# Performance work log

Measured on AMD Instinct MI355X. Metric: run time of the kernel, lower is better.

Reference implementation:

```python
import jax, jax.numpy as jnp
import numpy as np

B, S, D, H = 2, 2048, 768, 12
DK = D // H
NEG = -1000000000.0


def setup_inputs() -> dict:
    key = jax.random.key(0)
    ks = jax.random.split(key, 12)
    inp = {
        "query": jax.random.normal(ks[0], (B, S, D), jnp.float32),
        "key": jax.random.normal(ks[1], (B, S, D), jnp.float32),
        "value": jax.random.normal(ks[2], (B, S, D), jnp.float32),
        "mask": jax.random.randint(ks[3], (B, 1, 1, S), 0, 2, jnp.int32),
    }
    sc = 1.0 / np.sqrt(D)
    inp["Wq"] = jax.random.normal(ks[4], (D, D), jnp.float32) * sc
    inp["bq"] = jnp.zeros((D,), jnp.float32)
    inp["Wk"] = jax.random.normal(ks[5], (D, D), jnp.float32) * sc
    inp["bk"] = jnp.zeros((D,), jnp.float32)
    inp["Wv"] = jax.random.normal(ks[6], (D, D), jnp.float32) * sc
    inp["bv"] = jnp.zeros((D,), jnp.float32)
    inp["Wo"] = jax.random.normal(ks[7], (D, D), jnp.float32) * sc
    inp["bo"] = jnp.zeros((D,), jnp.float32)
    return inp


def reference(query, key, value, mask, Wq, bq, Wk, bk, Wv, bv, Wo, bo):
    b = query.shape[0]
    # QKV projections -> [B, H, S, DK]
    def proj(x, W, bias):
        y = jnp.einsum('bsd,de->bse', x, W.T) + bias
        return y.reshape(b, -1, H, DK).transpose(0, 2, 1, 3)
    q = proj(query, Wq, bq)
    k = proj(key, Wk, bk)
    v = proj(value, Wv, bv)
    # scores: [B, H, S, S]
    scores = jnp.einsum('bhqd,bhkd->bhqk', q, k) / jnp.sqrt(jnp.float32(DK))
    scores = jnp.where(mask == 0, jnp.float32(NEG), scores)
    p = jax.nn.softmax(scores, axis=-1)
    x = jnp.einsum('bhqk,bhkd->bhqd', p, v)  # [B, H, S, DK]
    x = x.transpose(0, 2, 1, 3).reshape(b, -1, H * DK)
    return jnp.einsum('bsd,de->bse', x, Wo.T) + bo
```

## Files before the change

kernel.cpp:

```cpp
#include <hip/hip_runtime.h>

typedef unsigned short u16;
typedef __attribute__((ext_vector_type(8))) __bf16 bf16x8;
typedef __attribute__((ext_vector_type(8))) short s16x8;
typedef __attribute__((ext_vector_type(8))) unsigned short u16x8;
typedef __attribute__((ext_vector_type(4))) float f32x4;
typedef __attribute__((ext_vector_type(4))) unsigned short u16x4;
typedef __attribute__((ext_vector_type(4))) float fl4;
typedef __attribute__((ext_vector_type(4))) int i32x4;
typedef __attribute__((ext_vector_type(4))) unsigned char u8x4;

#define MFMA(a, b, c) __builtin_amdgcn_mfma_f32_16x16x32_bf16((a), (b), (c), 0, 0, 0)
#define QSC 0.18033688011112042f

__device__ __forceinline__ u16 f2bf(float f) {
  __bf16 h = (__bf16)f;
  return __builtin_bit_cast(unsigned short, h);
}

__device__ __forceinline__ float bf2f(u16 u) {
  union { unsigned u; float f; } v; v.u = ((unsigned)u) << 16;
  return v.f;
}

__device__ __forceinline__ void gll16(const u16* g, u16* l) {
  typedef __attribute__((address_space(1))) unsigned int gu32;
  typedef __attribute__((address_space(3))) unsigned int lu32;
  __builtin_amdgcn_global_load_lds((gu32*)g, (lu32*)l, 16, 0, 0);
}


__global__ __launch_bounds__(256) void k_convert_w(
    const float* __restrict__ Wq, const float* __restrict__ Wk,
    const float* __restrict__ Wv, const float* __restrict__ Wo,
    u16* __restrict__ wqkv, u16* __restrict__ wob) {
  const int n = 3072 * 192;
  for (int i = blockIdx.x * 256 + threadIdx.x; i < n; i += gridDim.x * 256) {
    int row = i / 192;
    int col = (i - row * 192) * 4;
    const float* src; u16* dst; float sc = 1.0f;
    if (row < 768)       { src = Wq + row * 768;          dst = wqkv + row * 768; sc = QSC; }
    else if (row < 1536) { src = Wk + (row - 768) * 768;  dst = wqkv + row * 768; }
    else if (row < 2304) { src = Wv + (row - 1536) * 768; dst = wqkv + row * 768; }
    else                 { src = Wo + (row - 2304) * 768; dst = wob + (row - 2304) * 768; }
    fl4 f = *(const fl4*)(src + col);
    u16x4 o;
    o[0] = f2bf(f[0] * sc); o[1] = f2bf(f[1] * sc);
    o[2] = f2bf(f[2] * sc); o[3] = f2bf(f[3] * sc);
    *(u16x4*)(dst + col) = o;
  }
}


__global__ __launch_bounds__(256) void k_gemm_qkv(
    const float* __restrict__ xq, const float* __restrict__ xk,
    const float* __restrict__ xv, const u16* __restrict__ wqkv,
    const float* __restrict__ bq, const float* __restrict__ bk_,
    const float* __restrict__ bv_,
    u16* __restrict__ Qb, u16* __restrict__ Kb, u16* __restrict__ Vtb) {
  __shared__ __align__(16) u16 Abuf[2][128 * 32];
  __shared__ __align__(16) u16 Bbuf[2][128 * 32];
  const int tid = threadIdx.x;
  const int row0 = blockIdx.x * 128, col0 = blockIdx.y * 128;
  const int seg = col0 / 768;
  const float* A32 = (seg == 0) ? xq : ((seg == 1) ? xk : xv);
  const int w = tid >> 6, lane = tid & 63, lr = lane & 15, kg = lane >> 4;
  const int wr = (w >> 1) * 64, wc = (w & 1) * 64;

  const int c0 = tid, c1 = tid + 256;
  const int r0c = c0 >> 2, g0 = (c0 & 3) ^ ((r0c >> 1) & 3);
  const int r1c = c1 >> 2, g1 = (c1 & 3) ^ ((r1c >> 1) & 3);
  const float* aS0 = A32 + (size_t)(row0 + r0c) * 768 + g0 * 8;
  const float* aS1 = A32 + (size_t)(row0 + r1c) * 768 + g1 * 8;
  const u16* bS0 = wqkv + (size_t)(col0 + r0c) * 768 + g0 * 8;
  const u16* bS1 = wqkv + (size_t)(col0 + r1c) * 768 + g1 * 8;

  f32x4 acc[4][4];
  f32x4 zero = {0.f, 0.f, 0.f, 0.f};
#pragma unroll
  for (int i = 0; i < 4; i++)
#pragma unroll
    for (int j = 0; j < 4; j++) acc[i][j] = zero;

  int aoff[4], boff[4];
#pragma unroll
  for (int mi = 0; mi < 4; mi++) {
    int r = wr + mi * 16 + lr;
    aoff[mi] = r * 32 + (kg ^ ((r >> 1) & 3)) * 8;
  }
#pragma unroll
  for (int ni = 0; ni < 4; ni++) {
    int r = wc + ni * 16 + lr;
    boff[ni] = r * 32 + (kg ^ ((r >> 1) & 3)) * 8;
  }

  fl4 ar[4];
#define LOADA(kt) { ar[0] = *(const fl4*)(aS0 + (kt) * 32);       \
                    ar[1] = *(const fl4*)(aS0 + (kt) * 32 + 4);   \
                    ar[2] = *(const fl4*)(aS1 + (kt) * 32);       \
                    ar[3] = *(const fl4*)(aS1 + (kt) * 32 + 4); }
#define WRITEA(buf) { u16x8 t0, t1;                               \
    t0[0]=f2bf(ar[0][0]); t0[1]=f2bf(ar[0][1]); t0[2]=f2bf(ar[0][2]); t0[3]=f2bf(ar[0][3]); \
    t0[4]=f2bf(ar[1][0]); t0[5]=f2bf(ar[1][1]); t0[6]=f2bf(ar[1][2]); t0[7]=f2bf(ar[1][3]); \
    t1[0]=f2bf(ar[2][0]); t1[1]=f2bf(ar[2][1]); t1[2]=f2bf(ar[2][2]); t1[3]=f2bf(ar[2][3]); \
    t1[4]=f2bf(ar[3][0]); t1[5]=f2bf(ar[3][1]); t1[6]=f2bf(ar[3][2]); t1[7]=f2bf(ar[3][3]); \
    *(u16x8*)((buf) + c0 * 8) = t0; *(u16x8*)((buf) + c1 * 8) = t1; }
#define STAGEB(kt, buf) { gll16(bS0 + (kt) * 32, (buf) + c0 * 8); \
                          gll16(bS1 + (kt) * 32, (buf) + c1 * 8); }

  LOADA(0);
  STAGEB(0, Bbuf[0]);
  WRITEA(Abuf[0]);
  __syncthreads();

  for (int kt = 0; kt < 24; kt++) {
    const int cur = kt & 1;
    if (kt < 23) { LOADA(kt + 1); STAGEB(kt + 1, Bbuf[cur ^ 1]); }
    bf16x8 af[4], bfr[4];
#pragma unroll
    for (int mi = 0; mi < 4; mi++) af[mi] = *(const bf16x8*)(Abuf[cur] + aoff[mi]);
#pragma unroll
    for (int ni = 0; ni < 4; ni++) bfr[ni] = *(const bf16x8*)(Bbuf[cur] + boff[ni]);
#pragma unroll
    for (int mi = 0; mi < 4; mi++)
#pragma unroll
      for (int ni = 0; ni < 4; ni++)
        acc[mi][ni] = MFMA(af[mi], bfr[ni], acc[mi][ni]);
    if (kt < 23) WRITEA(Abuf[cur ^ 1]);
    __syncthreads();
  }
#undef LOADA
#undef WRITEA
#undef STAGEB

  const float* bias = (seg == 0) ? bq : ((seg == 1) ? bk_ : bv_);
  const float bsc = (seg == 0) ? QSC : 1.0f;
  const int ncol0 = col0 - seg * 768;
#pragma unroll
  for (int ni = 0; ni < 4; ni++) {
    const int n = ncol0 + wc + ni * 16 + lr;
    const float bval = bias[n] * bsc;
    const int hh = n >> 6, dk = n & 63;
#pragma unroll
    for (int mi = 0; mi < 4; mi++)
#pragma unroll
      for (int j = 0; j < 4; j++) {
        const int m = row0 + wr + mi * 16 + kg * 4 + j;
        const int bb = m >> 11, ss = m & 2047;
        const u16 val = f2bf(acc[mi][ni][j] + bval);
        if (seg == 0)
          Qb[((size_t)((bb * 12 + hh) * 2048 + ss)) * 64 + dk] = val;
        else if (seg == 1)
          Kb[((size_t)((bb * 12 + hh) * 2048 + ss)) * 64 + dk] = val;
        else
          Vtb[((size_t)((bb * 12 + hh) * 64 + dk)) * 2048 + ss] = val;
      }
  }
}


__global__ __launch_bounds__(256) void k_attn(
    const u16* __restrict__ Qb, const u16* __restrict__ Kb,
    const u16* __restrict__ Vtb, const int* __restrict__ mask,
    u16* __restrict__ o_part, float* __restrict__ l_part) {
  __shared__ __align__(16) u16 Ks[2][64 * 64];
  __shared__ __align__(16) u16 Vs[2][64 * 64];
  __shared__ __align__(16) u16 Ps[4][32 * 64];
  __shared__ __align__(4) unsigned char mlds8[1024];
  const int bid = blockIdx.x;
  const int wid = (bid & 7) * 96 + (bid >> 3);
  const int qt = wid & 15;
  const int gh = wid >> 4;
  const int bh = gh >> 1, half = gh & 1;
  const int b = bh / 12;
  const int kvb = half << 10;
  const int tid = threadIdx.x, w = tid >> 6, lane = tid & 63;
  const int lr = lane & 15, g = lane >> 4;
  const int q0 = qt * 128 + w * 32;
  const u16* Qh = Qb + (size_t)bh * (2048 * 64);
  const u16* Kh = Kb + (size_t)bh * (2048 * 64);
  const u16* Vh = Vtb + (size_t)bh * (64 * 2048);
  const int* mb = mask + b * 2048;
  u16* Pw = Ps[w];

  {
    i32x4 m4 = *(const i32x4*)(mb + kvb + tid * 4);
    u8x4 m8;
    m8[0] = (unsigned char)m4[0]; m8[1] = (unsigned char)m4[1];
    m8[2] = (unsigned char)m4[2]; m8[3] = (unsigned char)m4[3];
    *(u8x4*)(mlds8 + tid * 4) = m8;
  }

  bf16x8 aq[2][2];
#pragma unroll
  for (int mi = 0; mi < 2; mi++)
#pragma unroll
    for (int ks = 0; ks < 2; ks++)
      aq[mi][ks] = *(const bf16x8*)(Qh + (q0 + mi * 16 + lr) * 64 + ks * 32 + g * 8);

  f32x4 zero = {0.f, 0.f, 0.f, 0.f};
  f32x4 o[2][4];
#pragma unroll
  for (int mi = 0; mi < 2; mi++)
#pragma unroll
    for (int di = 0; di < 4; di++) o[mi][di] = zero;
  f32x4 o_l[2];
  o_l[0] = zero; o_l[1] = zero;

  s16x8 ov = {0x3F80, 0x3F80, 0x3F80, 0x3F80, 0x3F80, 0x3F80, 0x3F80, 0x3F80};
  bf16x8 ones = __builtin_bit_cast(bf16x8, ov);

  const int c0 = tid, c1 = tid + 256;
  const int sr0 = c0 >> 3, sg0 = (c0 & 7) ^ (sr0 & 7);
  const int sr1 = c1 >> 3, sg1 = (c1 & 7) ^ (sr1 & 7);
  const u16* kA0 = Kh + (size_t)kvb * 64 + sr0 * 64 + sg0 * 8;
  const u16* kA1 = Kh + (size_t)kvb * 64 + sr1 * 64 + sg1 * 8;
  const u16* vA0 = Vh + sr0 * 2048 + kvb + sg0 * 8;
  const u16* vA1 = Vh + sr1 * 2048 + kvb + sg1 * 8;

#define STAGE(u) { u16* kd = Ks[(u)&1]; u16* vd = Vs[(u)&1];           \
    gll16(kA0 + (u) * 4096, kd + c0 * 8);                              \
    gll16(kA1 + (u) * 4096, kd + c1 * 8);                              \
    gll16(vA0 + (u) * 64,  vd + c0 * 8);                               \
    gll16(vA1 + (u) * 64,  vd + c1 * 8); }

  STAGE(0);
  __syncthreads();

  for (int t = 0; t < 16; t++) {
    if (t < 15) STAGE(t + 1);
    const u16* Kc = Ks[t & 1];
    const u16* Vc = Vs[t & 1];

    f32x4 s[2][4];
#pragma unroll
    for (int ni = 0; ni < 4; ni++) {
      const int row = ni * 16 + lr;
      bf16x8 b0 = *(const bf16x8*)(Kc + row * 64 + ((g ^ (row & 7)) << 3));
      bf16x8 b1 = *(const bf16x8*)(Kc + row * 64 + (((4 + g) ^ (row & 7)) << 3));
#pragma unroll
      for (int mi = 0; mi < 2; mi++) {
        f32x4 z = MFMA(b0, aq[mi][0], zero);
        z = MFMA(b1, aq[mi][1], z);
        s[mi][ni] = z;
      }
    }
#pragma unroll
    for (int ni = 0; ni < 4; ni++) {
      const u8x4 mk4 = *(const u8x4*)(mlds8 + t * 64 + ni * 16 + g * 4);
#pragma unroll
      for (int mi = 0; mi < 2; mi++)
#pragma unroll
        for (int j = 0; j < 4; j++)
          s[mi][ni][j] = mk4[j] ? s[mi][ni][j] : -1e9f;
    }

#pragma unroll
    for (int mi = 0; mi < 2; mi++) {
      const int prow = mi * 16 + lr;
      const int rbase = prow * 128, sw = (prow & 7) << 4;
#pragma unroll
      for (int ni = 0; ni < 4; ni++) {
        u16x4 pk;
#pragma unroll
        for (int j = 0; j < 4; j++)
          pk[j] = f2bf(__builtin_amdgcn_exp2f(s[mi][ni][j]));
        *(u16x4*)(Pw + ((rbase + ((ni * 32 + g * 8) ^ sw)) >> 1)) = pk;
      }
    }

#pragma unroll
    for (int ks2 = 0; ks2 < 2; ks2++) {
      bf16x8 ap[2];
#pragma unroll
      for (int mi = 0; mi < 2; mi++) {
        const int prow = mi * 16 + lr;
        const int byt = prow * 128 + ((ks2 * 64 + g * 16) ^ ((prow & 7) << 4));
        ap[mi] = *(const bf16x8*)(Pw + (byt >> 1));
      }
#pragma unroll
      for (int di = 0; di < 4; di++) {
        const int vrow = di * 16 + lr;
        bf16x8 bv = *(const bf16x8*)(Vc + vrow * 64 + (((ks2 * 4 + g) ^ (vrow & 7)) << 3));
#pragma unroll
        for (int mi = 0; mi < 2; mi++)
          o[mi][di] = MFMA(ap[mi], bv, o[mi][di]);
      }
#pragma unroll
      for (int mi = 0; mi < 2; mi++)
        o_l[mi] = MFMA(ap[mi], ones, o_l[mi]);
    }

    if (t < 15) __syncthreads();
  }
#undef STAGE

  u16* opw = o_part + (size_t)(half * 24 + bh) * (2048 * 64);
  float* lpw = l_part + (size_t)(half * 24 + bh) * 2048;
#pragma unroll
  for (int mi = 0; mi < 2; mi++) {
#pragma unroll
    for (int di = 0; di < 4; di++)
#pragma unroll
      for (int j = 0; j < 4; j++) {
        const int row = q0 + mi * 16 + g * 4 + j;
        opw[(size_t)row * 64 + di * 16 + lr] = f2bf(o[mi][di][j]);
      }
    if (lr == 0) {
#pragma unroll
      for (int j = 0; j < 4; j++)
        lpw[q0 + mi * 16 + g * 4 + j] = o_l[mi][j];
    }
  }
}


__global__ __launch_bounds__(256) void k_combine(
    const u16* __restrict__ o_part, const float* __restrict__ l_part,
    u16* __restrict__ attn) {
  const int idx = blockIdx.x * 256 + threadIdx.x;
  const int row = idx >> 3;
  const int c8 = (idx & 7) << 3;
  const size_t HALF_O = (size_t)24 * 2048 * 64;
  u16x8 a0 = *(const u16x8*)(o_part + (size_t)row * 64 + c8);
  u16x8 a1 = *(const u16x8*)(o_part + HALF_O + (size_t)row * 64 + c8);
  const float l = l_part[row] + l_part[24 * 2048 + row];
  const float rcp = 1.0f / l;
  u16x8 r;
#pragma unroll
  for (int j = 0; j < 8; j++)
    r[j] = f2bf((bf2f(a0[j]) + bf2f(a1[j])) * rcp);
  const int bh = row >> 11, s = row & 2047;
  const int b = bh / 12, h = bh - b * 12;
  *(u16x8*)(attn + (size_t)(b * 2048 + s) * 768 + h * 64 + c8) = r;
}


__global__ __launch_bounds__(256) void k_gemm_out(
    const u16* __restrict__ attn, const u16* __restrict__ wob,
    const float* __restrict__ bo, float* __restrict__ out) {
  __shared__ __align__(16) u16 As[2][128 * 32];
  __shared__ __align__(16) u16 Bs[2][128 * 32];
  const int tid = threadIdx.x;
  const int bid = blockIdx.x;
  const int wid = (bid & 7) * 24 + (bid >> 3);
  const int row0 = (wid / 6) * 128, col0 = (wid % 6) * 128;
  const int w = tid >> 6, lane = tid & 63, lr = lane & 15, kg = lane >> 4;
  const int wr = (w >> 1) * 64, wc = (w & 1) * 64;

  const int c0 = tid, c1 = tid + 256;
  const int r0c = c0 >> 2, g0 = (c0 & 3) ^ ((r0c >> 1) & 3);
  const int r1c = c1 >> 2, g1 = (c1 & 3) ^ ((r1c >> 1) & 3);
  const u16* aS0 = attn + (size_t)(row0 + r0c) * 768 + g0 * 8;
  const u16* aS1 = attn + (size_t)(row0 + r1c) * 768 + g1 * 8;
  const u16* bS0 = wob + (size_t)(col0 + r0c) * 768 + g0 * 8;
  const u16* bS1 = wob + (size_t)(col0 + r1c) * 768 + g1 * 8;

  f32x4 acc[4][4];
  f32x4 zero = {0.f, 0.f, 0.f, 0.f};
#pragma unroll
  for (int i = 0; i < 4; i++)
#pragma unroll
    for (int j = 0; j < 4; j++) acc[i][j] = zero;

  int aoff[4], boff[4];
#pragma unroll
  for (int mi = 0; mi < 4; mi++) {
    int r = wr + mi * 16 + lr;
    aoff[mi] = r * 32 + (kg ^ ((r >> 1) & 3)) * 8;
  }
#pragma unroll
  for (int ni = 0; ni < 4; ni++) {
    int r = wc + ni * 16 + lr;
    boff[ni] = r * 32 + (kg ^ ((r >> 1) & 3)) * 8;
  }

#define STAGE(kt) { u16* ad = As[(kt)&1]; u16* bd = Bs[(kt)&1];   \
    gll16(aS0 + (kt) * 32, ad + c0 * 8);                          \
    gll16(aS1 + (kt) * 32, ad + c1 * 8);                          \
    gll16(bS0 + (kt) * 32, bd + c0 * 8);                          \
    gll16(bS1 + (kt) * 32, bd + c1 * 8); }

  STAGE(0);
  __syncthreads();

  for (int kt = 0; kt < 24; kt++) {
    const int cur = kt & 1;
    if (kt < 23) STAGE(kt + 1);
    bf16x8 af[4], bfr[4];
#pragma unroll
    for (int mi = 0; mi < 4; mi++) af[mi] = *(const bf16x8*)(As[cur] + aoff[mi]);
#pragma unroll
    for (int ni = 0; ni < 4; ni++) bfr[ni] = *(const bf16x8*)(Bs[cur] + boff[ni]);
#pragma unroll
    for (int mi = 0; mi < 4; mi++)
#pragma unroll
      for (int ni = 0; ni < 4; ni++)
        acc[mi][ni] = MFMA(af[mi], bfr[ni], acc[mi][ni]);
    if (kt < 23) __syncthreads();
  }
#undef STAGE

#pragma unroll
  for (int ni = 0; ni < 4; ni++) {
    const int n = col0 + wc + ni * 16 + lr;
    const float bval = bo[n];
#pragma unroll
    for (int mi = 0; mi < 4; mi++)
#pragma unroll
      for (int j = 0; j < 4; j++) {
        const int m = row0 + wr + mi * 16 + kg * 4 + j;
        out[(size_t)m * 768 + n] = acc[mi][ni][j] + bval;
      }
  }
}


extern "C" void kernel_launch(void* const* d_in, const int* in_sizes, int n_in,
                              void* d_out, int out_size, void* d_ws, size_t ws_size,
                              hipStream_t stream) {
  const float* q = (const float*)d_in[0];
  const float* k = (const float*)d_in[1];
  const float* v = (const float*)d_in[2];
  const int* mask = (const int*)d_in[3];
  const float* Wq = (const float*)d_in[4];
  const float* bq = (const float*)d_in[5];
  const float* Wk = (const float*)d_in[6];
  const float* bk = (const float*)d_in[7];
  const float* Wv = (const float*)d_in[8];
  const float* bv = (const float*)d_in[9];
  const float* Wo = (const float*)d_in[10];
  const float* bo = (const float*)d_in[11];
  float* out = (float*)d_out;

  u16* scratch = (u16*)d_ws;
  u16* wqkv = scratch + (size_t)3 * 4096 * 768;
  u16* wob = wqkv + (size_t)2304 * 768;
  u16* Qb = wob + (size_t)768 * 768;
  u16* Kb = Qb + (size_t)4096 * 768;
  u16* Vtb = Kb + (size_t)4096 * 768;
  u16* attn = Vtb + (size_t)4096 * 768;

  u16* o_part = scratch;
  float* l_part = (float*)(scratch + (size_t)2 * 24 * 2048 * 64);

  k_convert_w<<<dim3(2304), dim3(256), 0, stream>>>(Wq, Wk, Wv, Wo, wqkv, wob);
  k_gemm_qkv<<<dim3(32, 18), dim3(256), 0, stream>>>(q, k, v, wqkv, bq, bk, bv, Qb, Kb, Vtb);
  k_attn<<<dim3(768), dim3(256), 0, stream>>>(Qb, Kb, Vtb, mask, o_part, l_part);
  k_combine<<<dim3(1536), dim3(256), 0, stream>>>(o_part, l_part, attn);
  k_gemm_out<<<dim3(192), dim3(256), 0, stream>>>(attn, wob, bo, out);
}
```

Before: 106.3 us.

## Fuse split-K attention combine into output projection GEMM A-tile loading

Removes the separate combine kernel and the intermediate attn buffer. The output GEMM now reads both partial attention outputs and partial row sums directly, normalizes them in registers, and writes the bf16 A tile into shared memory. The B tile still goes through async global-to-LDS loads. This saves one launch and a round trip of the attention tensor through global memory. In exchange, the A tile is loaded through registers instead of async direct-to-LDS copies, and every column-block of the GEMM recomputes the combine for its rows (six times redundant).

```diff
diff --git a/kernel.cpp b/kernel.cpp
--- a/kernel.cpp
+++ b/kernel.cpp
@@ -315,29 +315,9 @@
 }
 
 
-__global__ __launch_bounds__(256) void k_combine(
+__global__ __launch_bounds__(256) void k_gemm_out(
     const u16* __restrict__ o_part, const float* __restrict__ l_part,
-    u16* __restrict__ attn) {
-  const int idx = blockIdx.x * 256 + threadIdx.x;
-  const int row = idx >> 3;
-  const int c8 = (idx & 7) << 3;
-  const size_t HALF_O = (size_t)24 * 2048 * 64;
-  u16x8 a0 = *(const u16x8*)(o_part + (size_t)row * 64 + c8);
-  u16x8 a1 = *(const u16x8*)(o_part + HALF_O + (size_t)row * 64 + c8);
-  const float l = l_part[row] + l_part[24 * 2048 + row];
-  const float rcp = 1.0f / l;
-  u16x8 r;
-#pragma unroll
-  for (int j = 0; j < 8; j++)
-    r[j] = f2bf((bf2f(a0[j]) + bf2f(a1[j])) * rcp);
-  const int bh = row >> 11, s = row & 2047;
-  const int b = bh / 12, h = bh - b * 12;
-  *(u16x8*)(attn + (size_t)(b * 2048 + s) * 768 + h * 64 + c8) = r;
-}
-
-
-__global__ __launch_bounds__(256) void k_gemm_out(
-    const u16* __restrict__ attn, const u16* __restrict__ wob,
+    const u16* __restrict__ wob,
     const float* __restrict__ bo, float* __restrict__ out) {
   __shared__ __align__(16) u16 As[2][128 * 32];
   __shared__ __align__(16) u16 Bs[2][128 * 32];
@@ -351,8 +331,15 @@
   const int c0 = tid, c1 = tid + 256;
   const int r0c = c0 >> 2, g0 = (c0 & 3) ^ ((r0c >> 1) & 3);
   const int r1c = c1 >> 2, g1 = (c1 & 3) ^ ((r1c >> 1) & 3);
-  const u16* aS0 = attn + (size_t)(row0 + r0c) * 768 + g0 * 8;
-  const u16* aS1 = attn + (size_t)(row0 + r1c) * 768 + g1 * 8;
+  const int m0 = row0 + r0c, m1 = row0 + r1c;
+  const int bb0 = m0 >> 11, ss0 = m0 & 2047;
+  const int bb1 = m1 >> 11, ss1 = m1 & 2047;
+  const size_t obase0 = (size_t)(bb0 * 12) * 131072 + (size_t)ss0 * 64;
+  const size_t obase1 = (size_t)(bb1 * 12) * 131072 + (size_t)ss1 * 64;
+  const int lb0 = bb0 * 12 * 2048 + ss0;
+  const int lb1 = bb1 * 12 * 2048 + ss1;
+  const size_t HALF_O = (size_t)24 * 2048 * 64;
+  const int LHALF = 24 * 2048;
   const u16* bS0 = wob + (size_t)(col0 + r0c) * 768 + g0 * 8;
   const u16* bS1 = wob + (size_t)(col0 + r1c) * 768 + g1 * 8;
 
@@ -375,18 +362,49 @@
     boff[ni] = r * 32 + (kg ^ ((r >> 1) & 3)) * 8;
   }
 
-#define STAGE(kt) { u16* ad = As[(kt)&1]; u16* bd = Bs[(kt)&1];   \
-    gll16(aS0 + (kt) * 32, ad + c0 * 8);                          \
-    gll16(aS1 + (kt) * 32, ad + c1 * 8);                          \
-    gll16(bS0 + (kt) * 32, bd + c0 * 8);                          \
-    gll16(bS1 + (kt) * 32, bd + c1 * 8); }
-
-  STAGE(0);
+  u16x8 ca0, ca0h, ca1, ca1h;
+  float cl0, cl0h, cl1, cl1h;
+#define LOADC(kt) { const int hh = (kt) >> 1;                                   \
+    const int dk0 = ((kt) & 1) * 32 + g0 * 8, dk1 = ((kt) & 1) * 32 + g1 * 8;   \
+    const size_t o0 = obase0 + (size_t)hh * 131072 + dk0;                       \
+    const size_t o1 = obase1 + (size_t)hh * 131072 + dk1;                       \
+    ca0  = *(const u16x8*)(o_part + o0);                                        \
+    ca0h = *(const u16x8*)(o_part + HALF_O + o0);                               \
+    ca1  = *(const u16x8*)(o_part + o1);                                        \
+    ca1h = *(const u16x8*)(o_part + HALF_O + o1);                               \
+    cl0 = l_part[lb0 + hh * 2048]; cl0h = l_part[LHALF + lb0 + hh * 2048];      \
+    cl1 = l_part[lb1 + hh * 2048]; cl1h = l_part[LHALF + lb1 + hh * 2048]; }
+#define WRITEC(buf) { const float rcp0 = 1.0f / (cl0 + cl0h);                   \
+    const float rcp1 = 1.0f / (cl1 + cl1h);                                     \
+    u16x8 t0, t1;                                                               \
+    t0[0]=f2bf((bf2f(ca0[0])+bf2f(ca0h[0]))*rcp0);                              \
+    t0[1]=f2bf((bf2f(ca0[1])+bf2f(ca0h[1]))*rcp0);                              \
+    t0[2]=f2bf((bf2f(ca0[2])+bf2f(ca0h[2]))*rcp0);                              \
+    t0[3]=f2bf((bf2f(ca0[3])+bf2f(ca0h[3]))*rcp0);                              \
+    t0[4]=f2bf((bf2f(ca0[4])+bf2f(ca0h[4]))*rcp0);                              \
+    t0[5]=f2bf((bf2f(ca0[5])+bf2f(ca0h[5]))*rcp0);                              \
+    t0[6]=f2bf((bf2f(ca0[6])+bf2f(ca0h[6]))*rcp0);                              \
+    t0[7]=f2bf((bf2f(ca0[7])+bf2f(ca0h[7]))*rcp0);                              \
+    t1[0]=f2bf((bf2f(ca1[0])+bf2f(ca1h[0]))*rcp1);                              \
+    t1[1]=f2bf((bf2f(ca1[1])+bf2f(ca1h[1]))*rcp1);                              \
+    t1[2]=f2bf((bf2f(ca1[2])+bf2f(ca1h[2]))*rcp1);                              \
+    t1[3]=f2bf((bf2f(ca1[3])+bf2f(ca1h[3]))*rcp1);                              \
+    t1[4]=f2bf((bf2f(ca1[4])+bf2f(ca1h[4]))*rcp1);                              \
+    t1[5]=f2bf((bf2f(ca1[5])+bf2f(ca1h[5]))*rcp1);                              \
+    t1[6]=f2bf((bf2f(ca1[6])+bf2f(ca1h[6]))*rcp1);                              \
+    t1[7]=f2bf((bf2f(ca1[7])+bf2f(ca1h[7]))*rcp1);                              \
+    *(u16x8*)((buf) + c0 * 8) = t0; *(u16x8*)((buf) + c1 * 8) = t1; }
+#define STAGEB(kt, buf) { gll16(bS0 + (kt) * 32, (buf) + c0 * 8); \
+                          gll16(bS1 + (kt) * 32, (buf) + c1 * 8); }
+
+  LOADC(0);
+  STAGEB(0, Bs[0]);
+  WRITEC(As[0]);
   __syncthreads();
 
   for (int kt = 0; kt < 24; kt++) {
     const int cur = kt & 1;
-    if (kt < 23) STAGE(kt + 1);
+    if (kt < 23) { LOADC(kt + 1); STAGEB(kt + 1, Bs[cur ^ 1]); }
     bf16x8 af[4], bfr[4];
 #pragma unroll
     for (int mi = 0; mi < 4; mi++) af[mi] = *(const bf16x8*)(As[cur] + aoff[mi]);
@@ -397,9 +415,12 @@
 #pragma unroll
       for (int ni = 0; ni < 4; ni++)
         acc[mi][ni] = MFMA(af[mi], bfr[ni], acc[mi][ni]);
-    if (kt < 23) __syncthreads();
-  }
-#undef STAGE
+    if (kt < 23) WRITEC(As[cur ^ 1]);
+    __syncthreads();
+  }
+#undef LOADC
+#undef WRITEC
+#undef STAGEB
 
 #pragma unroll
   for (int ni = 0; ni < 4; ni++) {
@@ -439,7 +460,6 @@
   u16* Qb = wob + (size_t)768 * 768;
   u16* Kb = Qb + (size_t)4096 * 768;
   u16* Vtb = Kb + (size_t)4096 * 768;
-  u16* attn = Vtb + (size_t)4096 * 768;
 
   u16* o_part = scratch;
   float* l_part = (float*)(scratch + (size_t)2 * 24 * 2048 * 64);
@@ -447,6 +467,5 @@
   k_convert_w<<<dim3(2304), dim3(256), 0, stream>>>(Wq, Wk, Wv, Wo, wqkv, wob);
   k_gemm_qkv<<<dim3(32, 18), dim3(256), 0, stream>>>(q, k, v, wqkv, bq, bk, bv, Qb, Kb, Vtb);
   k_attn<<<dim3(768), dim3(256), 0, stream>>>(Qb, Kb, Vtb, mask, o_part, l_part);
-  k_combine<<<dim3(1536), dim3(256), 0, stream>>>(o_part, l_part, attn);
-  k_gemm_out<<<dim3(192), dim3(256), 0, stream>>>(attn, wob, bo, out);
-}
+  k_gemm_out<<<dim3(192), dim3(256), 0, stream>>>(o_part, l_part, wob, bo, out);
+}
```

New measurement: 114.9 us. 8.1% more time.
